# Optimization experiments

Hardware: AMD Instinct MI355X
Metric: run time of the kernel (lower is better)

## Reference

```python
import jax, jax.numpy as jnp
import numpy as np

N = 50000      # nodes
E = 800000     # edges
D_IN = 128
D_H = 128
D_OUT = 64


def setup_inputs() -> dict:
    key = jax.random.key(0)
    ks = jax.random.split(key, 10)
    x = jax.random.normal(ks[0], (N, D_IN), dtype=jnp.float32)
    edge_index = jax.random.randint(ks[1], (2, E), 0, N, dtype=jnp.int32)
    def glorot(k, fan_in, fan_out):
        s = jnp.sqrt(6.0 / (fan_in + fan_out)).astype(jnp.float32)
        return jax.random.uniform(k, (fan_in, fan_out), jnp.float32, -s, s)
    return {
        "x": x,
        "edge_index": edge_index,
        "W1": glorot(ks[2], D_IN, D_H), "b1": jnp.zeros((D_H,), jnp.float32),
        "W2": glorot(ks[3], D_H, D_H),  "b2": jnp.zeros((D_H,), jnp.float32),
        "W3": glorot(ks[4], D_H, D_H),  "b3": jnp.zeros((D_H,), jnp.float32),
        "Wfc": glorot(ks[5], D_H, D_OUT), "bfc": jnp.zeros((D_OUT,), jnp.float32),
    }


def gcn_conv(x, W, b, src, dst, n):
    h = x @ W                                   # [N, d_out]
    loop = jnp.arange(n, dtype=src.dtype)
    src_f = jnp.concatenate([src, loop])        # [E+N]
    dst_f = jnp.concatenate([dst, loop])
    deg = jax.ops.segment_sum(jnp.ones_like(dst_f, dtype=h.dtype), dst_f, num_segments=n)
    dinv = jnp.where(deg > 0, jax.lax.rsqrt(deg), 0.0)
    norm = dinv[src_f] * dinv[dst_f]            # [E+N]
    msgs = h[src_f] * norm[:, None]             # gather + scale
    out = jax.ops.segment_sum(msgs, dst_f, num_segments=n)  # scatter-add
    return out + b


def reference(x, edge_index, W1, b1, W2, b2, W3, b3, Wfc, bfc):
    src, dst = edge_index[0], edge_index[1]
    n = x.shape[0]
    h = x
    for W, b in ((W1, b1), (W2, b2), (W3, b3)):
        h = jax.nn.relu(gcn_conv(h, W, b, src, dst, n))
    # dropout is identity in eval mode
    return h @ Wfc + bfc
```

## Files before the change

### kernel.cpp

```cpp
#include <hip/hip_runtime.h>
#include <hip/hip_bf16.h>

#define NN 50000
#define EE 800000
#define DD 128
#define DOUTC 64
#define CAP 64

typedef unsigned int uint;
typedef unsigned short ushort;
typedef __attribute__((ext_vector_type(8))) short bf16x8;
typedef __attribute__((ext_vector_type(4))) float f32x4;

__device__ __forceinline__ float bf2f(uint b) { return __uint_as_float(b << 16); }
__device__ __forceinline__ ushort f2bf(float f) {
    uint u = __float_as_uint(f);
    u += 0x7fffu + ((u >> 16) & 1u);
    return (ushort)(u >> 16);
}

__global__ __launch_bounds__(256) void k_detect(const uint* __restrict__ x,
                                                int* __restrict__ flag) {
    __shared__ int sh[256];
    int t = threadIdx.x;
    int c = 0;
    for (int i = 0; i < 16; ++i) {
        uint e = (x[t * 16 + i] >> 7) & 0xFFu;
        c += (e >= 118u && e <= 132u) ? 1 : 0;
    }
    sh[t] = c;
    __syncthreads();
    for (int o = 128; o > 0; o >>= 1) {
        if (t < o) sh[t] += sh[t + o];
        __syncthreads();
    }
    if (t == 0) flag[0] = (sh[0] > 2048) ? 1 : 0;
}

__global__ void k_prep_x(const void* __restrict__ x, ushort* __restrict__ xb,
                         const int* __restrict__ flag) {
    int i = blockIdx.x * blockDim.x + threadIdx.x;
    size_t base = (size_t)i * 8;
    if (base >= (size_t)NN * DD) return;
    if (flag[0]) {
        ((uint4*)xb)[i] = ((const uint4*)x)[i];
    } else {
        const float* xf = (const float*)x + base;
        float4 a = *(const float4*)xf;
        float4 b = *(const float4*)(xf + 4);
        uint4 o;
        o.x = (uint)f2bf(a.x) | ((uint)f2bf(a.y) << 16);
        o.y = (uint)f2bf(a.z) | ((uint)f2bf(a.w) << 16);
        o.z = (uint)f2bf(b.x) | ((uint)f2bf(b.y) << 16);
        o.w = (uint)f2bf(b.z) | ((uint)f2bf(b.w) << 16);
        ((uint4*)xb)[i] = o;
    }
}

struct PrepW {
    const void *w1, *w2, *w3, *wfc, *b1, *b2, *b3, *bfc;
    ushort *wt1, *wt2, *wt3, *wtfc, *bb1, *bb2, *bb3, *bbfc;
};

__device__ __forceinline__ ushort ld_bf(const void* p, int idx, bool bf) {
    return bf ? ((const ushort*)p)[idx] : f2bf(((const float*)p)[idx]);
}

__global__ __launch_bounds__(256) void k_prep_w(PrepW a, const int* __restrict__ flag) {
    const bool bf = flag[0] != 0;
    int b = blockIdx.x, t = threadIdx.x;
    if (b < 192) {
        const void* w = (b < 64) ? a.w1 : (b < 128) ? a.w2 : a.w3;
        ushort* wt = (b < 64) ? a.wt1 : (b < 128) ? a.wt2 : a.wt3;
        int idx = (b & 63) * 256 + t;
        int k = idx >> 7, n = idx & 127;
        wt[n * DD + k] = ld_bf(w, idx, bf);
    } else if (b < 224) {
        int idx = (b - 192) * 256 + t;
        int k = idx >> 6, n = idx & 63;
        a.wtfc[n * DD + k] = ld_bf(a.wfc, idx, bf);
    } else {
        const void* s = (b == 224) ? a.b1 : (b == 225) ? a.b2 : (b == 226) ? a.b3 : a.bfc;
        ushort* d = (b == 224) ? a.bb1 : (b == 225) ? a.bb2 : (b == 226) ? a.bb3 : a.bbfc;
        int len = (b == 227) ? DOUTC : DD;
        if (t < len) d[t] = ld_bf(s, t, bf);
    }
}

__global__ void k_zero(int* __restrict__ cnt) {
    int i = blockIdx.x * blockDim.x + threadIdx.x;
    if (i < NN) cnt[i] = 0;
}

__global__ void k_bucket(const int* __restrict__ src, const int* __restrict__ dst,
                         int* __restrict__ cnt, int* __restrict__ colb) {
    int e = blockIdx.x * blockDim.x + threadIdx.x;
    if (e < EE) {
        int d = dst[e];
        int p = atomicAdd(&cnt[d], 1);
        if (p < CAP) colb[((size_t)d << 6) + p] = src[e];
    }
}

__global__ void k_dinv(const int* __restrict__ cnt, float* __restrict__ dinv) {
    int i = blockIdx.x * blockDim.x + threadIdx.x;
    if (i < NN) dinv[i] = rsqrtf((float)(cnt[i] + 1));
}


__global__ __launch_bounds__(256) void k_mm(
    const ushort* __restrict__ H, const ushort* __restrict__ WT,
    const float* __restrict__ dinv, ushort* __restrict__ T) {
    const int wave = threadIdx.x >> 6;
    const int lane = threadIdx.x & 63;
    const int m0w = blockIdx.x * 64 + wave * 16;
    if (m0w >= NN) return;
    const int m = m0w + (lane & 15);
    const int quad = lane >> 4;
    f32x4 acc[8];
#pragma unroll
    for (int nt = 0; nt < 8; ++nt) acc[nt] = (f32x4){0.f, 0.f, 0.f, 0.f};
    const ushort* Hrow = H + (size_t)m * DD;
#pragma unroll
    for (int kk = 0; kk < 4; ++kk) {
        bf16x8 bfr = *(const bf16x8*)(Hrow + kk * 32 + quad * 8);
#pragma unroll
        for (int nt = 0; nt < 8; ++nt) {
            bf16x8 afr = *(const bf16x8*)(WT + (size_t)(nt * 16 + (lane & 15)) * DD +
                                          kk * 32 + quad * 8);
            acc[nt] = __builtin_amdgcn_mfma_f32_16x16x32_bf16(afr, bfr, acc[nt], 0, 0, 0);
        }
    }
    const float di = dinv[m];
#pragma unroll
    for (int nt = 0; nt < 8; ++nt) {
        int n = nt * 16 + quad * 4;
        uint2 o;
        o.x = (uint)f2bf(acc[nt][0] * di) | ((uint)f2bf(acc[nt][1] * di) << 16);
        o.y = (uint)f2bf(acc[nt][2] * di) | ((uint)f2bf(acc[nt][3] * di) << 16);
        *(uint2*)(T + (size_t)m * DD + n) = o;
    }
}

__global__ __launch_bounds__(256) void k_mm_final(
    const ushort* __restrict__ H, const ushort* __restrict__ WT,
    const ushort* __restrict__ bb, void* __restrict__ out_,
    const int* __restrict__ flag) {
    const int wave = threadIdx.x >> 6;
    const int lane = threadIdx.x & 63;
    const int m0w = blockIdx.x * 64 + wave * 16;
    if (m0w >= NN) return;
    const int m = m0w + (lane & 15);
    const int quad = lane >> 4;
    f32x4 acc[4];
#pragma unroll
    for (int nt = 0; nt < 4; ++nt) acc[nt] = (f32x4){0.f, 0.f, 0.f, 0.f};
    const ushort* Hrow = H + (size_t)m * DD;
#pragma unroll
    for (int kk = 0; kk < 4; ++kk) {
        bf16x8 bfr = *(const bf16x8*)(Hrow + kk * 32 + quad * 8);
#pragma unroll
        for (int nt = 0; nt < 4; ++nt) {
            bf16x8 afr = *(const bf16x8*)(WT + (size_t)(nt * 16 + (lane & 15)) * DD +
                                          kk * 32 + quad * 8);
            acc[nt] = __builtin_amdgcn_mfma_f32_16x16x32_bf16(afr, bfr, acc[nt], 0, 0, 0);
        }
    }
    const bool bf = flag[0] != 0;
#pragma unroll
    for (int nt = 0; nt < 4; ++nt) {
        int n = nt * 16 + quad * 4;
        float b0 = bf2f((uint)bb[n]), b1 = bf2f((uint)bb[n + 1]);
        float b2 = bf2f((uint)bb[n + 2]), b3 = bf2f((uint)bb[n + 3]);
        float v0 = acc[nt][0] + b0, v1 = acc[nt][1] + b1;
        float v2 = acc[nt][2] + b2, v3 = acc[nt][3] + b3;
        if (bf) {
            uint2 o;
            o.x = (uint)f2bf(v0) | ((uint)f2bf(v1) << 16);
            o.y = (uint)f2bf(v2) | ((uint)f2bf(v3) << 16);
            *(uint2*)((ushort*)out_ + (size_t)m * DOUTC + n) = o;
        } else {
            float4 o = {v0, v1, v2, v3};
            *(float4*)((float*)out_ + (size_t)m * DOUTC + n) = o;
        }
    }
}

__global__ __launch_bounds__(256) void k_agg(
    const ushort* __restrict__ T, const int* __restrict__ cnt,
    const int* __restrict__ colb, const float* __restrict__ dinv,
    const ushort* __restrict__ bb, ushort* __restrict__ A) {
    int node = blockIdx.x * 4 + (threadIdx.x >> 6);
    if (node >= NN) return;
    int lane = threadIdx.x & 63;
    const uint* Tv = (const uint*)T;
    size_t base = (size_t)node * 64;
    uint w0 = Tv[base + lane];
    float ax = bf2f(w0 & 0xffffu), ay = bf2f(w0 >> 16);
    int c = cnt[node];
    int end = c < CAP ? c : CAP;
    const int* bl = colb + ((size_t)node << 6);
    int e = 0;
    for (; e + 3 < end; e += 4) {
        int s0 = bl[e], s1 = bl[e + 1], s2 = bl[e + 2], s3 = bl[e + 3];
        uint v0 = Tv[(size_t)s0 * 64 + lane];
        uint v1 = Tv[(size_t)s1 * 64 + lane];
        uint v2 = Tv[(size_t)s2 * 64 + lane];
        uint v3 = Tv[(size_t)s3 * 64 + lane];
        ax += (bf2f(v0 & 0xffffu) + bf2f(v1 & 0xffffu)) +
              (bf2f(v2 & 0xffffu) + bf2f(v3 & 0xffffu));
        ay += (bf2f(v0 >> 16) + bf2f(v1 >> 16)) + (bf2f(v2 >> 16) + bf2f(v3 >> 16));
    }
    for (; e < end; ++e) {
        uint v = Tv[(size_t)bl[e] * 64 + lane];
        ax += bf2f(v & 0xffffu);
        ay += bf2f(v >> 16);
    }
    float di = dinv[node];
    uint bw = ((const uint*)bb)[lane];
    float o0 = fmaxf(fmaf(ax, di, bf2f(bw & 0xffffu)), 0.f);
    float o1 = fmaxf(fmaf(ay, di, bf2f(bw >> 16)), 0.f);
    ((uint*)A)[base + lane] = (uint)f2bf(o0) | ((uint)f2bf(o1) << 16);
}

extern "C" void kernel_launch(void* const* d_in, const int* in_sizes, int n_in,
                              void* d_out, int out_size, void* d_ws, size_t ws_size,
                              hipStream_t stream) {
    const void* x   = d_in[0];
    const int*  ei  = (const int*)d_in[1];

    char* ws = (char*)d_ws;
    size_t off = 0;
    auto take = [&](size_t bytes) {
        void* p = ws + off;
        off = (off + bytes + 255) & ~(size_t)255;
        return p;
    };
    int*    flag = (int*)take(4);
    int*    cnt  = (int*)take((size_t)NN * 4);
    int*    colb = (int*)take((size_t)NN * CAP * 4);
    float*  dinv = (float*)take((size_t)NN * 4);
    ushort* Xb   = (ushort*)take((size_t)NN * DD * 2);
    ushort* T    = (ushort*)take((size_t)NN * DD * 2);
    ushort* A    = (ushort*)take((size_t)NN * DD * 2);
    ushort* WT1  = (ushort*)take((size_t)DD * DD * 2);
    ushort* WT2  = (ushort*)take((size_t)DD * DD * 2);
    ushort* WT3  = (ushort*)take((size_t)DD * DD * 2);
    ushort* WTfc = (ushort*)take((size_t)DOUTC * DD * 2);
    ushort* bb1  = (ushort*)take(DD * 2);
    ushort* bb2  = (ushort*)take(DD * 2);
    ushort* bb3  = (ushort*)take(DD * 2);
    ushort* bbfc = (ushort*)take(DOUTC * 2);

    const int* src = ei;
    const int* dst = ei + EE;

    k_detect<<<1, 256, 0, stream>>>((const uint*)x, flag);

    PrepW pw;
    pw.w1 = d_in[2]; pw.b1 = d_in[3];
    pw.w2 = d_in[4]; pw.b2 = d_in[5];
    pw.w3 = d_in[6]; pw.b3 = d_in[7];
    pw.wfc = d_in[8]; pw.bfc = d_in[9];
    pw.wt1 = WT1; pw.wt2 = WT2; pw.wt3 = WT3; pw.wtfc = WTfc;
    pw.bb1 = bb1; pw.bb2 = bb2; pw.bb3 = bb3; pw.bbfc = bbfc;

    k_prep_x<<<(NN * DD / 8 + 255) / 256, 256, 0, stream>>>(x, Xb, flag);
    k_prep_w<<<228, 256, 0, stream>>>(pw, flag);
    k_zero<<<(NN + 255) / 256, 256, 0, stream>>>(cnt);
    k_bucket<<<(EE + 255) / 256, 256, 0, stream>>>(src, dst, cnt, colb);
    k_dinv<<<(NN + 255) / 256, 256, 0, stream>>>(cnt, dinv);

    const int mm_grid  = (NN + 63) / 64;
    const int agg_grid = (NN + 3) / 4;

    k_mm<<<mm_grid, 256, 0, stream>>>(Xb, WT1, dinv, T);
    k_agg<<<agg_grid, 256, 0, stream>>>(T, cnt, colb, dinv, bb1, A);
    k_mm<<<mm_grid, 256, 0, stream>>>(A, WT2, dinv, T);
    k_agg<<<agg_grid, 256, 0, stream>>>(T, cnt, colb, dinv, bb2, A);
    k_mm<<<mm_grid, 256, 0, stream>>>(A, WT3, dinv, T);
    k_agg<<<agg_grid, 256, 0, stream>>>(T, cnt, colb, dinv, bb3, A);
    k_mm_final<<<mm_grid, 256, 0, stream>>>(A, WTfc, bbfc, d_out, flag);
}
```

Measured before the change: 349.8 us.

## Fuse preprocessing kernels, merge bucketing with first GEMM, compress neighbor lists

```diff
diff --git a/kernel.cpp b/kernel.cpp
--- a/kernel.cpp
+++ b/kernel.cpp
@@ -1,11 +1,11 @@
 #include <hip/hip_runtime.h>
-#include <hip/hip_bf16.h>
 
 #define NN 50000
 #define EE 800000
 #define DD 128
 #define DOUTC 64
 #define CAP 64
+#define BUCKET_BLKS 3125
 
 typedef unsigned int uint;
 typedef unsigned short ushort;
@@ -19,98 +19,86 @@
     return (ushort)(u >> 16);
 }
 
-__global__ __launch_bounds__(256) void k_detect(const uint* __restrict__ x,
-                                                int* __restrict__ flag) {
-    __shared__ int sh[256];
-    int t = threadIdx.x;
-    int c = 0;
-    for (int i = 0; i < 16; ++i) {
-        uint e = (x[t * 16 + i] >> 7) & 0xFFu;
-        c += (e >= 118u && e <= 132u) ? 1 : 0;
-    }
-    sh[t] = c;
-    __syncthreads();
-    for (int o = 128; o > 0; o >>= 1) {
-        if (t < o) sh[t] += sh[t + o];
-        __syncthreads();
-    }
-    if (t == 0) flag[0] = (sh[0] > 2048) ? 1 : 0;
-}
-
-__global__ void k_prep_x(const void* __restrict__ x, ushort* __restrict__ xb,
-                         const int* __restrict__ flag) {
-    int i = blockIdx.x * blockDim.x + threadIdx.x;
-    size_t base = (size_t)i * 8;
-    if (base >= (size_t)NN * DD) return;
-    if (flag[0]) {
-        ((uint4*)xb)[i] = ((const uint4*)x)[i];
+struct PreArgs {
+    const float *w1, *w2, *w3, *wfc;
+    ushort *wt1, *wt2, *wt3, *wtfc;
+    int* cnt;
+};
+
+__global__ __launch_bounds__(256) void k_pre(PreArgs a) {
+    int b = blockIdx.x, t = threadIdx.x;
+    if (b < 196) {
+        int i = b * 256 + t;
+        if (i < NN) a.cnt[i] = 0;
+    } else if (b < 388) {
+        int b2 = b - 196;
+        const float* w = (b2 < 64) ? a.w1 : (b2 < 128) ? a.w2 : a.w3;
+        ushort* wt = (b2 < 64) ? a.wt1 : (b2 < 128) ? a.wt2 : a.wt3;
+        int idx = (b2 & 63) * 256 + t;
+        int k = idx >> 7, n = idx & 127;
+        wt[n * DD + k] = f2bf(w[idx]);
     } else {
-        const float* xf = (const float*)x + base;
-        float4 a = *(const float4*)xf;
-        float4 b = *(const float4*)(xf + 4);
-        uint4 o;
-        o.x = (uint)f2bf(a.x) | ((uint)f2bf(a.y) << 16);
-        o.y = (uint)f2bf(a.z) | ((uint)f2bf(a.w) << 16);
-        o.z = (uint)f2bf(b.x) | ((uint)f2bf(b.y) << 16);
-        o.w = (uint)f2bf(b.z) | ((uint)f2bf(b.w) << 16);
-        ((uint4*)xb)[i] = o;
-    }
-}
-
-struct PrepW {
-    const void *w1, *w2, *w3, *wfc, *b1, *b2, *b3, *bfc;
-    ushort *wt1, *wt2, *wt3, *wtfc, *bb1, *bb2, *bb3, *bbfc;
-};
-
-__device__ __forceinline__ ushort ld_bf(const void* p, int idx, bool bf) {
-    return bf ? ((const ushort*)p)[idx] : f2bf(((const float*)p)[idx]);
-}
-
-__global__ __launch_bounds__(256) void k_prep_w(PrepW a, const int* __restrict__ flag) {
-    const bool bf = flag[0] != 0;
-    int b = blockIdx.x, t = threadIdx.x;
-    if (b < 192) {
-        const void* w = (b < 64) ? a.w1 : (b < 128) ? a.w2 : a.w3;
-        ushort* wt = (b < 64) ? a.wt1 : (b < 128) ? a.wt2 : a.wt3;
-        int idx = (b & 63) * 256 + t;
-        int k = idx >> 7, n = idx & 127;
-        wt[n * DD + k] = ld_bf(w, idx, bf);
-    } else if (b < 224) {
-        int idx = (b - 192) * 256 + t;
+        int idx = (b - 388) * 256 + t;
         int k = idx >> 6, n = idx & 63;
-        a.wtfc[n * DD + k] = ld_bf(a.wfc, idx, bf);
-    } else {
-        const void* s = (b == 224) ? a.b1 : (b == 225) ? a.b2 : (b == 226) ? a.b3 : a.bfc;
-        ushort* d = (b == 224) ? a.bb1 : (b == 225) ? a.bb2 : (b == 226) ? a.bb3 : a.bbfc;
-        int len = (b == 227) ? DOUTC : DD;
-        if (t < len) d[t] = ld_bf(s, t, bf);
-    }
-}
-
-__global__ void k_zero(int* __restrict__ cnt) {
-    int i = blockIdx.x * blockDim.x + threadIdx.x;
-    if (i < NN) cnt[i] = 0;
-}
-
-__global__ void k_bucket(const int* __restrict__ src, const int* __restrict__ dst,
-                         int* __restrict__ cnt, int* __restrict__ colb) {
-    int e = blockIdx.x * blockDim.x + threadIdx.x;
-    if (e < EE) {
+        a.wtfc[n * DD + k] = f2bf(a.wfc[idx]);
+    }
+}
+
+
+__global__ __launch_bounds__(256) void k_front(
+    const int* __restrict__ src, const int* __restrict__ dst,
+    int* __restrict__ cnt, ushort* __restrict__ colb,
+    const float* __restrict__ X, const ushort* __restrict__ WT1,
+    ushort* __restrict__ T) {
+    int b = blockIdx.x;
+    if (b < BUCKET_BLKS) {
+        int e = b * 256 + threadIdx.x;
         int d = dst[e];
+        int s = src[e];
         int p = atomicAdd(&cnt[d], 1);
-        if (p < CAP) colb[((size_t)d << 6) + p] = src[e];
-    }
-}
-
-__global__ void k_dinv(const int* __restrict__ cnt, float* __restrict__ dinv) {
-    int i = blockIdx.x * blockDim.x + threadIdx.x;
-    if (i < NN) dinv[i] = rsqrtf((float)(cnt[i] + 1));
-}
-
+        if (p < CAP) colb[((size_t)d << 6) + p] = (ushort)s;
+        return;
+    }
+    const int mb = b - BUCKET_BLKS;
+    const int wave = threadIdx.x >> 6;
+    const int lane = threadIdx.x & 63;
+    const int m0w = mb * 64 + wave * 16;
+    if (m0w >= NN) return;
+    const int m = m0w + (lane & 15);
+    const int quad = lane >> 4;
+    f32x4 acc[8];
+#pragma unroll
+    for (int nt = 0; nt < 8; ++nt) acc[nt] = (f32x4){0.f, 0.f, 0.f, 0.f};
+    const float* Hrow = X + (size_t)m * DD;
+#pragma unroll
+    for (int kk = 0; kk < 4; ++kk) {
+        float4 a0 = *(const float4*)(Hrow + kk * 32 + quad * 8);
+        float4 a1 = *(const float4*)(Hrow + kk * 32 + quad * 8 + 4);
+        bf16x8 bfr;
+        bfr[0] = (short)f2bf(a0.x); bfr[1] = (short)f2bf(a0.y);
+        bfr[2] = (short)f2bf(a0.z); bfr[3] = (short)f2bf(a0.w);
+        bfr[4] = (short)f2bf(a1.x); bfr[5] = (short)f2bf(a1.y);
+        bfr[6] = (short)f2bf(a1.z); bfr[7] = (short)f2bf(a1.w);
+#pragma unroll
+        for (int nt = 0; nt < 8; ++nt) {
+            bf16x8 afr = *(const bf16x8*)(WT1 + (size_t)(nt * 16 + (lane & 15)) * DD +
+                                          kk * 32 + quad * 8);
+            acc[nt] = __builtin_amdgcn_mfma_f32_16x16x32_bf16(afr, bfr, acc[nt], 0, 0, 0);
+        }
+    }
+#pragma unroll
+    for (int nt = 0; nt < 8; ++nt) {
+        int n = nt * 16 + quad * 4;
+        uint2 o;
+        o.x = (uint)f2bf(acc[nt][0]) | ((uint)f2bf(acc[nt][1]) << 16);
+        o.y = (uint)f2bf(acc[nt][2]) | ((uint)f2bf(acc[nt][3]) << 16);
+        *(uint2*)(T + (size_t)m * DD + n) = o;
+    }
+}
 
 __global__ __launch_bounds__(256) void k_mm(
     const ushort* __restrict__ H, const ushort* __restrict__ WT,
-    const float* __restrict__ dinv, ushort* __restrict__ T) {
+    ushort* __restrict__ T) {
     const int wave = threadIdx.x >> 6;
     const int lane = threadIdx.x & 63;
     const int m0w = blockIdx.x * 64 + wave * 16;
@@ -131,21 +119,67 @@
             acc[nt] = __builtin_amdgcn_mfma_f32_16x16x32_bf16(afr, bfr, acc[nt], 0, 0, 0);
         }
     }
-    const float di = dinv[m];
 #pragma unroll
     for (int nt = 0; nt < 8; ++nt) {
         int n = nt * 16 + quad * 4;
         uint2 o;
-        o.x = (uint)f2bf(acc[nt][0] * di) | ((uint)f2bf(acc[nt][1] * di) << 16);
-        o.y = (uint)f2bf(acc[nt][2] * di) | ((uint)f2bf(acc[nt][3] * di) << 16);
+        o.x = (uint)f2bf(acc[nt][0]) | ((uint)f2bf(acc[nt][1]) << 16);
+        o.y = (uint)f2bf(acc[nt][2]) | ((uint)f2bf(acc[nt][3]) << 16);
         *(uint2*)(T + (size_t)m * DD + n) = o;
     }
+}
+
+__global__ __launch_bounds__(256) void k_agg(
+    const ushort* __restrict__ T, const int* __restrict__ cnt,
+    const ushort* __restrict__ colb, const float* __restrict__ bias,
+    ushort* __restrict__ A) {
+    int node = blockIdx.x * 4 + (threadIdx.x >> 6);
+    if (node >= NN) return;
+    int lane = threadIdx.x & 63;
+    const uint* Tv = (const uint*)T;
+    size_t base = (size_t)node * 64;
+    int c = cnt[node];
+    float di = rsqrtf((float)(c + 1));
+    uint w0 = Tv[base + lane];
+    float ax = di * bf2f(w0 & 0xffffu), ay = di * bf2f(w0 >> 16);
+    int end = c < CAP ? c : CAP;
+    const ushort* bl = colb + ((size_t)node << 6);
+    int e = 0;
+    for (; e + 3 < end; e += 4) {
+        int s0 = bl[e], s1 = bl[e + 1], s2 = bl[e + 2], s3 = bl[e + 3];
+        float d0 = rsqrtf((float)(cnt[s0] + 1));
+        float d1 = rsqrtf((float)(cnt[s1] + 1));
+        float d2 = rsqrtf((float)(cnt[s2] + 1));
+        float d3 = rsqrtf((float)(cnt[s3] + 1));
+        uint v0 = Tv[(size_t)s0 * 64 + lane];
+        uint v1 = Tv[(size_t)s1 * 64 + lane];
+        uint v2 = Tv[(size_t)s2 * 64 + lane];
+        uint v3 = Tv[(size_t)s3 * 64 + lane];
+        ax = fmaf(d0, bf2f(v0 & 0xffffu), ax);
+        ay = fmaf(d0, bf2f(v0 >> 16), ay);
+        ax = fmaf(d1, bf2f(v1 & 0xffffu), ax);
+        ay = fmaf(d1, bf2f(v1 >> 16), ay);
+        ax = fmaf(d2, bf2f(v2 & 0xffffu), ax);
+        ay = fmaf(d2, bf2f(v2 >> 16), ay);
+        ax = fmaf(d3, bf2f(v3 & 0xffffu), ax);
+        ay = fmaf(d3, bf2f(v3 >> 16), ay);
+    }
+    for (; e < end; ++e) {
+        int s = bl[e];
+        float dj = rsqrtf((float)(cnt[s] + 1));
+        uint v = Tv[(size_t)s * 64 + lane];
+        ax = fmaf(dj, bf2f(v & 0xffffu), ax);
+        ay = fmaf(dj, bf2f(v >> 16), ay);
+    }
+    float2 bv = ((const float2*)bias)[lane];
+    float o0 = fmaxf(fmaf(ax, di, bv.x), 0.f);
+    float o1 = fmaxf(fmaf(ay, di, bv.y), 0.f);
+    ((uint*)A)[base + lane] = (uint)f2bf(o0) | ((uint)f2bf(o1) << 16);
 }
 
 __global__ __launch_bounds__(256) void k_mm_final(
     const ushort* __restrict__ H, const ushort* __restrict__ WT,
-    const ushort* __restrict__ bb, void* __restrict__ out_,
-    const int* __restrict__ flag) {
+    const float* __restrict__ bb, float* __restrict__ out) {
     const int wave = threadIdx.x >> 6;
     const int lane = threadIdx.x & 63;
     const int m0w = blockIdx.x * 64 + wave * 16;
@@ -166,68 +200,29 @@
             acc[nt] = __builtin_amdgcn_mfma_f32_16x16x32_bf16(afr, bfr, acc[nt], 0, 0, 0);
         }
     }
-    const bool bf = flag[0] != 0;
 #pragma unroll
     for (int nt = 0; nt < 4; ++nt) {
         int n = nt * 16 + quad * 4;
-        float b0 = bf2f((uint)bb[n]), b1 = bf2f((uint)bb[n + 1]);
-        float b2 = bf2f((uint)bb[n + 2]), b3 = bf2f((uint)bb[n + 3]);
-        float v0 = acc[nt][0] + b0, v1 = acc[nt][1] + b1;
-        float v2 = acc[nt][2] + b2, v3 = acc[nt][3] + b3;
-        if (bf) {
-            uint2 o;
-            o.x = (uint)f2bf(v0) | ((uint)f2bf(v1) << 16);
-            o.y = (uint)f2bf(v2) | ((uint)f2bf(v3) << 16);
-            *(uint2*)((ushort*)out_ + (size_t)m * DOUTC + n) = o;
-        } else {
-            float4 o = {v0, v1, v2, v3};
-            *(float4*)((float*)out_ + (size_t)m * DOUTC + n) = o;
-        }
-    }
-}
-
-__global__ __launch_bounds__(256) void k_agg(
-    const ushort* __restrict__ T, const int* __restrict__ cnt,
-    const int* __restrict__ colb, const float* __restrict__ dinv,
-    const ushort* __restrict__ bb, ushort* __restrict__ A) {
-    int node = blockIdx.x * 4 + (threadIdx.x >> 6);
-    if (node >= NN) return;
-    int lane = threadIdx.x & 63;
-    const uint* Tv = (const uint*)T;
-    size_t base = (size_t)node * 64;
-    uint w0 = Tv[base + lane];
-    float ax = bf2f(w0 & 0xffffu), ay = bf2f(w0 >> 16);
-    int c = cnt[node];
-    int end = c < CAP ? c : CAP;
-    const int* bl = colb + ((size_t)node << 6);
-    int e = 0;
-    for (; e + 3 < end; e += 4) {
-        int s0 = bl[e], s1 = bl[e + 1], s2 = bl[e + 2], s3 = bl[e + 3];
-        uint v0 = Tv[(size_t)s0 * 64 + lane];
-        uint v1 = Tv[(size_t)s1 * 64 + lane];
-        uint v2 = Tv[(size_t)s2 * 64 + lane];
-        uint v3 = Tv[(size_t)s3 * 64 + lane];
-        ax += (bf2f(v0 & 0xffffu) + bf2f(v1 & 0xffffu)) +
-              (bf2f(v2 & 0xffffu) + bf2f(v3 & 0xffffu));
-        ay += (bf2f(v0 >> 16) + bf2f(v1 >> 16)) + (bf2f(v2 >> 16) + bf2f(v3 >> 16));
-    }
-    for (; e < end; ++e) {
-        uint v = Tv[(size_t)bl[e] * 64 + lane];
-        ax += bf2f(v & 0xffffu);
-        ay += bf2f(v >> 16);
-    }
-    float di = dinv[node];
-    uint bw = ((const uint*)bb)[lane];
-    float o0 = fmaxf(fmaf(ax, di, bf2f(bw & 0xffffu)), 0.f);
-    float o1 = fmaxf(fmaf(ay, di, bf2f(bw >> 16)), 0.f);
-    ((uint*)A)[base + lane] = (uint)f2bf(o0) | ((uint)f2bf(o1) << 16);
+        float4 bvals = *(const float4*)(bb + n);
+        float4 o = {acc[nt][0] + bvals.x, acc[nt][1] + bvals.y,
+                    acc[nt][2] + bvals.z, acc[nt][3] + bvals.w};
+        *(float4*)(out + (size_t)m * DOUTC + n) = o;
+    }
 }
 
 extern "C" void kernel_launch(void* const* d_in, const int* in_sizes, int n_in,
                               void* d_out, int out_size, void* d_ws, size_t ws_size,
                               hipStream_t stream) {
-    const void* x   = d_in[0];
-    const int*  ei  = (const int*)d_in[1];
+    const float* x   = (const float*)d_in[0];
+    const int*   ei  = (const int*)d_in[1];
+    const float* W1  = (const float*)d_in[2];
+    const float* b1  = (const float*)d_in[3];
+    const float* W2  = (const float*)d_in[4];
+    const float* b2  = (const float*)d_in[5];
+    const float* W3  = (const float*)d_in[6];
+    const float* b3  = (const float*)d_in[7];
+    const float* Wfc = (const float*)d_in[8];
+    const float* bfc = (const float*)d_in[9];
 
     char* ws = (char*)d_ws;
     size_t off = 0;
@@ -236,49 +231,32 @@
         off = (off + bytes + 255) & ~(size_t)255;
         return p;
     };
-    int*    flag = (int*)take(4);
     int*    cnt  = (int*)take((size_t)NN * 4);
-    int*    colb = (int*)take((size_t)NN * CAP * 4);
-    float*  dinv = (float*)take((size_t)NN * 4);
-    ushort* Xb   = (ushort*)take((size_t)NN * DD * 2);
+    ushort* colb = (ushort*)take((size_t)NN * CAP * 2);
     ushort* T    = (ushort*)take((size_t)NN * DD * 2);
     ushort* A    = (ushort*)take((size_t)NN * DD * 2);
     ushort* WT1  = (ushort*)take((size_t)DD * DD * 2);
     ushort* WT2  = (ushort*)take((size_t)DD * DD * 2);
     ushort* WT3  = (ushort*)take((size_t)DD * DD * 2);
     ushort* WTfc = (ushort*)take((size_t)DOUTC * DD * 2);
-    ushort* bb1  = (ushort*)take(DD * 2);
-    ushort* bb2  = (ushort*)take(DD * 2);
-    ushort* bb3  = (ushort*)take(DD * 2);
-    ushort* bbfc = (ushort*)take(DOUTC * 2);
 
     const int* src = ei;
     const int* dst = ei + EE;
 
-    k_detect<<<1, 256, 0, stream>>>((const uint*)x, flag);
-
-    PrepW pw;
-    pw.w1 = d_in[2]; pw.b1 = d_in[3];
-    pw.w2 = d_in[4]; pw.b2 = d_in[5];
-    pw.w3 = d_in[6]; pw.b3 = d_in[7];
-    pw.wfc = d_in[8]; pw.bfc = d_in[9];
-    pw.wt1 = WT1; pw.wt2 = WT2; pw.wt3 = WT3; pw.wtfc = WTfc;
-    pw.bb1 = bb1; pw.bb2 = bb2; pw.bb3 = bb3; pw.bbfc = bbfc;
-
-    k_prep_x<<<(NN * DD / 8 + 255) / 256, 256, 0, stream>>>(x, Xb, flag);
-    k_prep_w<<<228, 256, 0, stream>>>(pw, flag);
-    k_zero<<<(NN + 255) / 256, 256, 0, stream>>>(cnt);
-    k_bucket<<<(EE + 255) / 256, 256, 0, stream>>>(src, dst, cnt, colb);
-    k_dinv<<<(NN + 255) / 256, 256, 0, stream>>>(cnt, dinv);
+    PreArgs pa;
+    pa.w1 = W1; pa.w2 = W2; pa.w3 = W3; pa.wfc = Wfc;
+    pa.wt1 = WT1; pa.wt2 = WT2; pa.wt3 = WT3; pa.wtfc = WTfc;
+    pa.cnt = cnt;
+    k_pre<<<420, 256, 0, stream>>>(pa);
 
     const int mm_grid  = (NN + 63) / 64;
     const int agg_grid = (NN + 3) / 4;
 
-    k_mm<<<mm_grid, 256, 0, stream>>>(Xb, WT1, dinv, T);
-    k_agg<<<agg_grid, 256, 0, stream>>>(T, cnt, colb, dinv, bb1, A);
-    k_mm<<<mm_grid, 256, 0, stream>>>(A, WT2, dinv, T);
-    k_agg<<<agg_grid, 256, 0, stream>>>(T, cnt, colb, dinv, bb2, A);
-    k_mm<<<mm_grid, 256, 0, stream>>>(A, WT3, dinv, T);
-    k_agg<<<agg_grid, 256, 0, stream>>>(T, cnt, colb, dinv, bb3, A);
-    k_mm_final<<<mm_grid, 256, 0, stream>>>(A, WTfc, bbfc, d_out, flag);
-}
+    k_front<<<BUCKET_BLKS + mm_grid, 256, 0, stream>>>(src, dst, cnt, colb, x, WT1, T);
+    k_agg<<<agg_grid, 256, 0, stream>>>(T, cnt, colb, b1, A);
+    k_mm<<<mm_grid, 256, 0, stream>>>(A, WT2, T);
+    k_agg<<<agg_grid, 256, 0, stream>>>(T, cnt, colb, b2, A);
+    k_mm<<<mm_grid, 256, 0, stream>>>(A, WT3, T);
+    k_agg<<<agg_grid, 256, 0, stream>>>(T, cnt, colb, b3, A);
+    k_mm_final<<<mm_grid, 256, 0, stream>>>(A, WTfc, bfc, (float*)d_out);
+}
```

After: 352.2 us. Within noise of the previous version (+0.7%).
